# Kernel optimization log

Hardware: AMD Instinct MI355X
Metric: run time of the kernel (lower is better)

Reference implementation:

```python
import jax, jax.numpy as jnp
import numpy as np

THRESH = 0.85

def setup_inputs() -> dict:
    key = jax.random.key(0)
    k1, k2 = jax.random.split(key)
    bs, d, r, c = 4, 16, 64, 64
    n = r * c
    seg = jax.random.normal(k1, (bs, d, r, c), dtype=jnp.float32)
    W = jax.random.uniform(k2, (bs, n, n), dtype=jnp.float32)
    return {"seg": seg, "W": W}

def reference(seg, W):
    bs, d, r, c = seg.shape
    # threshold affinity: keep values > 0.85
    Wt = jnp.where(W > THRESH, W, jnp.zeros((), W.dtype))
    # row-normalize: D = diag(1/rowsum(Wt)) @ Wt  (broadcast division)
    D = Wt / Wt.sum(axis=-1, keepdims=True)          # [bs, n, n]
    seg_flat = seg.reshape(bs, d, r * c)             # [bs, d, n]
    # seg_flat @ D^T : out[b,d,m] = sum_n seg[b,d,n] * D[b,m,n]
    out = jnp.einsum('bdn,bmn->bdm', seg_flat, D)
    return out.reshape(bs, d, r, c)
```

## Files before the change

### kernel.cpp

```cpp
#include <hip/hip_runtime.h>


typedef float v4f __attribute__((ext_vector_type(4)));

#define N_DIM 4096
#define D_DIM 16
#define THRESH 0.85f
#define RPW 2
#define CHUNK 256
#define NCHUNK (N_DIM / CHUNK)

__global__ __launch_bounds__(256) void regu_kernel(
    const float* __restrict__ seg,
    const float* __restrict__ W,
    float* __restrict__ out)
{
    const int lane = threadIdx.x & 63;
    const int wv   = threadIdx.x >> 6;
    const int gwave = blockIdx.x * 4 + wv;
    const int row0  = gwave * RPW;
    const int b  = row0 >> 12;
    const int m0 = row0 & (N_DIM - 1);

    const float* Wp   = W   + ((size_t)b * N_DIM + m0) * N_DIM + lane * 4;
    const float* segp = seg + (size_t)b * D_DIM * N_DIM + lane * 4;

    float acc[RPW * D_DIM];
    float rowsum[RPW] = {0.f, 0.f};
#pragma unroll
    for (int i = 0; i < RPW * D_DIM; ++i) acc[i] = 0.f;

    v4f buf0[RPW], buf1[RPW];
#pragma unroll
    for (int r = 0; r < RPW; ++r)
        buf0[r] = __builtin_nontemporal_load((const v4f*)(Wp + (size_t)r * N_DIM));

    auto compute = [&](const v4f* wb, int c) {
        v4f w[RPW];
#pragma unroll
        for (int r = 0; r < RPW; ++r) {
            v4f v = wb[r];
            v.x = (v.x > THRESH) ? v.x : 0.f;
            v.y = (v.y > THRESH) ? v.y : 0.f;
            v.z = (v.z > THRESH) ? v.z : 0.f;
            v.w = (v.w > THRESH) ? v.w : 0.f;
            w[r] = v;
            rowsum[r] += (v.x + v.y) + (v.z + v.w);
        }
        const float* sp = segp + c * CHUNK;
#pragma unroll
        for (int d = 0; d < D_DIM; ++d) {
            const v4f s = *(const v4f*)(sp + d * N_DIM);
#pragma unroll
            for (int r = 0; r < RPW; ++r) {
                acc[r * D_DIM + d] += w[r].x * s.x;
                acc[r * D_DIM + d] += w[r].y * s.y;
                acc[r * D_DIM + d] += w[r].z * s.z;
                acc[r * D_DIM + d] += w[r].w * s.w;
            }
        }
    };

    for (int c = 0; c < NCHUNK; c += 2) {
        {
            const float* p = Wp + (size_t)(c + 1) * CHUNK;
#pragma unroll
            for (int r = 0; r < RPW; ++r)
                buf1[r] = __builtin_nontemporal_load((const v4f*)(p + (size_t)r * N_DIM));
        }
        compute(buf0, c);

        if (c + 2 < NCHUNK) {
            const float* p = Wp + (size_t)(c + 2) * CHUNK;
#pragma unroll
            for (int r = 0; r < RPW; ++r)
                buf0[r] = __builtin_nontemporal_load((const v4f*)(p + (size_t)r * N_DIM));
        }
        compute(buf1, c + 1);
    }

#pragma unroll
    for (int k = 0; k < 5; ++k) {
        const int S = 16 >> k;
        const bool up = (lane >> k) & 1;
#pragma unroll
        for (int j = 0; j < S; ++j) {
            const float mine = up ? acc[j + S] : acc[j];
            const float send = up ? acc[j] : acc[j + S];
            acc[j] = mine + __shfl_xor(send, 1 << k, 64);
        }
    }
    acc[0] += __shfl_xor(acc[0], 32, 64);

#pragma unroll
    for (int r = 0; r < RPW; ++r) {
        float s = rowsum[r];
#pragma unroll
        for (int off = 1; off < 64; off <<= 1) s += __shfl_xor(s, off, 64);
        rowsum[r] = s;
    }

    if (lane < 32) {
        const int j = __brev((unsigned)lane) >> 27;
        const int r = j >> 4;
        const int d = j & 15;
        const float inv = 1.0f / (r ? rowsum[1] : rowsum[0]);
        out[((size_t)b * D_DIM + d) * N_DIM + (m0 + r)] = acc[0] * inv;
    }
}

extern "C" void kernel_launch(void* const* d_in, const int* in_sizes, int n_in,
                              void* d_out, int out_size, void* d_ws, size_t ws_size,
                              hipStream_t stream) {
    const float* seg = (const float*)d_in[0];
    const float* W   = (const float*)d_in[1];
    float* out = (float*)d_out;

    regu_kernel<<<2048, 256, 0, stream>>>(seg, W, out);
}
```

Baseline: 405.0 us.

## Stage seg chunks in LDS via async global_load_lds and double rows per wave

Each block now cooperatively copies the current seg chunk into a double-buffered shared-memory tile with global_load_lds. All four waves read that tile instead of each fetching seg from global or L2 on their own. Rows per wave go from 2 to 4, which halves the grid and gives each seg value more reuse; the butterfly reduction gains one level to match. This cuts seg re-reads, which had been a large part of memory traffic beside the streaming W reads, but adds block-wide barriers each chunk and more accumulator registers, which may lower occupancy.

```diff
diff --git a/kernel.cpp b/kernel.cpp
--- a/kernel.cpp
+++ b/kernel.cpp
@@ -1,4 +1,5 @@
 #include <hip/hip_runtime.h>
+#include <stdint.h>
 
 
 typedef float v4f __attribute__((ext_vector_type(4)));
@@ -6,7 +7,7 @@
 #define N_DIM 4096
 #define D_DIM 16
 #define THRESH 0.85f
-#define RPW 2
+#define RPW 4
 #define CHUNK 256
 #define NCHUNK (N_DIM / CHUNK)
 
@@ -15,31 +16,48 @@
     const float* __restrict__ W,
     float* __restrict__ out)
 {
+    __shared__ float stile[2][D_DIM * CHUNK];
+
     const int lane = threadIdx.x & 63;
     const int wv   = threadIdx.x >> 6;
-    const int gwave = blockIdx.x * 4 + wv;
-    const int row0  = gwave * RPW;
+    const int row0 = blockIdx.x * 16 + wv * RPW;
     const int b  = row0 >> 12;
     const int m0 = row0 & (N_DIM - 1);
 
     const float* Wp   = W   + ((size_t)b * N_DIM + m0) * N_DIM + lane * 4;
-    const float* segp = seg + (size_t)b * D_DIM * N_DIM + lane * 4;
+    const float* segb = seg + (size_t)b * D_DIM * N_DIM;
 
     float acc[RPW * D_DIM];
-    float rowsum[RPW] = {0.f, 0.f};
+    float rowsum[RPW] = {0.f, 0.f, 0.f, 0.f};
 #pragma unroll
     for (int i = 0; i < RPW * D_DIM; ++i) acc[i] = 0.f;
 
-    v4f buf0[RPW], buf1[RPW];
+#define STAGE(c, sb)                                                          \
+    do {                                                                      \
+        _Pragma("unroll")                                                     \
+        for (int j = 0; j < 4; ++j) {                                         \
+            const int d_ = wv * 4 + j;                                        \
+            const float* g_ = segb + (size_t)d_ * N_DIM + (c) * CHUNK + lane * 4; \
+            __builtin_amdgcn_global_load_lds(                                 \
+                (const __attribute__((address_space(1))) uint32_t*)g_,        \
+                (__attribute__((address_space(3))) uint32_t*)&stile[sb][d_ * CHUNK], \
+                16, 0, 0);                                                    \
+        }                                                                     \
+    } while (0)
+
+    v4f wA[RPW], wB[RPW];
+
+    STAGE(0, 0);
 #pragma unroll
     for (int r = 0; r < RPW; ++r)
-        buf0[r] = __builtin_nontemporal_load((const v4f*)(Wp + (size_t)r * N_DIM));
+        wA[r] = __builtin_nontemporal_load((const v4f*)(Wp + (size_t)r * N_DIM));
+    __syncthreads();
 
-    auto compute = [&](const v4f* wb, int c) {
+    auto compute = [&](const v4f* w_in, int sb) {
         v4f w[RPW];
 #pragma unroll
         for (int r = 0; r < RPW; ++r) {
-            v4f v = wb[r];
+            v4f v = w_in[r];
             v.x = (v.x > THRESH) ? v.x : 0.f;
             v.y = (v.y > THRESH) ? v.y : 0.f;
             v.z = (v.z > THRESH) ? v.z : 0.f;
@@ -47,10 +65,9 @@
             w[r] = v;
             rowsum[r] += (v.x + v.y) + (v.z + v.w);
         }
-        const float* sp = segp + c * CHUNK;
 #pragma unroll
         for (int d = 0; d < D_DIM; ++d) {
-            const v4f s = *(const v4f*)(sp + d * N_DIM);
+            const v4f s = *(const v4f*)&stile[sb][d * CHUNK + lane * 4];
 #pragma unroll
             for (int r = 0; r < RPW; ++r) {
                 acc[r * D_DIM + d] += w[r].x * s.x;
@@ -62,26 +79,30 @@
     };
 
     for (int c = 0; c < NCHUNK; c += 2) {
+        STAGE(c + 1, 1);
         {
             const float* p = Wp + (size_t)(c + 1) * CHUNK;
 #pragma unroll
             for (int r = 0; r < RPW; ++r)
-                buf1[r] = __builtin_nontemporal_load((const v4f*)(p + (size_t)r * N_DIM));
+                wB[r] = __builtin_nontemporal_load((const v4f*)(p + (size_t)r * N_DIM));
         }
-        compute(buf0, c);
+        compute(wA, 0);
+        __syncthreads();
 
         if (c + 2 < NCHUNK) {
+            STAGE(c + 2, 0);
             const float* p = Wp + (size_t)(c + 2) * CHUNK;
 #pragma unroll
             for (int r = 0; r < RPW; ++r)
-                buf0[r] = __builtin_nontemporal_load((const v4f*)(p + (size_t)r * N_DIM));
+                wA[r] = __builtin_nontemporal_load((const v4f*)(p + (size_t)r * N_DIM));
         }
-        compute(buf1, c + 1);
+        compute(wB, 1);
+        __syncthreads();
     }
 
 #pragma unroll
-    for (int k = 0; k < 5; ++k) {
-        const int S = 16 >> k;
+    for (int k = 0; k < 6; ++k) {
+        const int S = 32 >> k;
         const bool up = (lane >> k) & 1;
 #pragma unroll
         for (int j = 0; j < S; ++j) {
@@ -90,7 +111,6 @@
             acc[j] = mine + __shfl_xor(send, 1 << k, 64);
         }
     }
-    acc[0] += __shfl_xor(acc[0], 32, 64);
 
 #pragma unroll
     for (int r = 0; r < RPW; ++r) {
@@ -100,13 +120,12 @@
         rowsum[r] = s;
     }
 
-    if (lane < 32) {
-        const int j = __brev((unsigned)lane) >> 27;
-        const int r = j >> 4;
-        const int d = j & 15;
-        const float inv = 1.0f / (r ? rowsum[1] : rowsum[0]);
-        out[((size_t)b * D_DIM + d) * N_DIM + (m0 + r)] = acc[0] * inv;
-    }
+    const int j = __brev((unsigned)lane) >> 26;
+    const int r = j >> 4;
+    const int d = j & 15;
+    const float inv = 1.0f / (r < 2 ? (r == 0 ? rowsum[0] : rowsum[1])
+                                    : (r == 2 ? rowsum[2] : rowsum[3]));
+    out[((size_t)b * D_DIM + d) * N_DIM + (m0 + r)] = acc[0] * inv;
 }
 
 extern "C" void kernel_launch(void* const* d_in, const int* in_sizes, int n_in,
@@ -116,5 +135,5 @@
     const float* W   = (const float*)d_in[1];
     float* out = (float*)d_out;
 
-    regu_kernel<<<2048, 256, 0, stream>>>(seg, W, out);
+    regu_kernel<<<1024, 256, 0, stream>>>(seg, W, out);
 }
```

Measured after the change: 354.3 us. 12.5% less time.
